# Kernel tuning notes

Hardware: AMD Instinct MI355X
Metric: run time of the kernel (lower is better)

## Reference

```python
import jax, jax.numpy as jnp
import numpy as np

NEG_SLOPE = 0.01  # torch nn.LeakyReLU default
N_NODES, N_EDGES, N_BATCH, L_PATH = 100000, 300000, 50000, 4
D_EMB, D_HID, N_HEADS = 128, 64, 8


def setup_inputs() -> dict:
    key = jax.random.key(0)
    ks = jax.random.split(key, 10)
    return {
        "batch_nodes": jax.random.randint(ks[0], (N_BATCH,), 0, N_NODES),
        "metapath_indices": jax.random.randint(ks[1], (N_EDGES, L_PATH), 0, N_NODES),
        "edge_dst": jax.random.randint(ks[2], (N_EDGES,), 0, N_NODES),
        "transformed_feature": jax.random.normal(ks[3], (N_NODES, D_EMB), jnp.float32),
        "W_i": jax.random.normal(ks[4], (D_HID, D_EMB), jnp.float32) * 0.05,
        "W_p": jax.random.normal(ks[5], (D_HID, D_EMB), jnp.float32) * 0.05,
        "attn": jax.random.normal(ks[6], (1, N_HEADS, D_HID), jnp.float32) * 0.05,
        "W_th": jax.random.normal(ks[7], (N_HEADS, N_HEADS), jnp.float32) * 0.3,
        "W_gate": jax.random.normal(ks[8], (1, D_HID), jnp.float32) * 0.1,
        "b_gate": jnp.zeros((1,), jnp.float32),
    }


def reference(batch_nodes, metapath_indices, edge_dst, transformed_feature,
              W_i, W_p, attn, W_th, W_gate, b_gate):
    N = transformed_feature.shape[0]
    # node_type_specific_agg for mtype==1: h_src/h_dst through linear_i, h_p1/h_p2 through linear_p
    membd = transformed_feature[metapath_indices]                      # [E, 4, D_emb]
    edata = (membd[:, 0] + membd[:, 3]) @ W_i.T \
          + (membd[:, 1] + membd[:, 2]) @ W_p.T                        # [E, D]
    E, D = edata.shape
    H = attn.shape[1]
    # cat([edata]*H, dim=1).view(-1, H, D) duplicates edata per head
    efeat = jnp.broadcast_to(edata[:, None, :], (E, H, D))             # [E, H, D]
    # talking-heads attention logits, leaky-relu
    logits = (efeat * attn).sum(-1) @ W_th.T                           # [E, H]
    logits = jax.nn.leaky_relu(logits, NEG_SLOPE)
    # dgl edge_softmax: per-dst-node, per-head softmax over incoming edges (stable)
    m = jax.ops.segment_max(logits, edge_dst, num_segments=N)          # [N, H]
    ex = jnp.exp(logits - m[edge_dst])                                 # [E, H]
    den = jax.ops.segment_sum(ex, edge_dst, num_segments=N)            # [N, H]
    a = ex / den[edge_dst]                                             # [E, H]  (dropout rate 0)
    # message passing: ft = efeature * a, summed per dst node
    msgs = (efeat * a[:, :, None]).reshape(E, H * D)
    node_ft = jax.ops.segment_sum(msgs, edge_dst, num_segments=N)      # [N, H*D]
    result = node_ft[batch_nodes].reshape(-1, H, D)                    # [B, H, D]
    # gated multi-head attention: gate = mean over batch of fc_gate(result)
    gate = jnp.mean(result @ W_gate.T + b_gate, axis=0)                # [H, 1]
    result = result * gate[None]                                       # [B, H, D]
    return result.reshape(-1, H * D)
```

## Files before the change

### kernel.cpp

```cpp
#include <hip/hip_runtime.h>
#include <cstdint>
#include <cstddef>


typedef __attribute__((ext_vector_type(8))) short bf16x8;
typedef __attribute__((ext_vector_type(4))) float f32x4;
typedef __attribute__((ext_vector_type(8))) unsigned short u16x8;

__device__ __forceinline__ unsigned short f2bf(float f) {
    unsigned u = __float_as_uint(f);
    unsigned r = u + 0x7fffu + ((u >> 16) & 1u);
    return (unsigned short)(r >> 16);
}
__device__ __forceinline__ float bf2f(unsigned short h) {
    return __uint_as_float((unsigned)h << 16);
}
__device__ __forceinline__ unsigned fenc(float f) {
    unsigned u = __float_as_uint(f);
    return (u & 0x80000000u) ? ~u : (u | 0x80000000u);
}
__device__ __forceinline__ float fdec(unsigned k) {
    unsigned u = (k & 0x80000000u) ? (k & 0x7fffffffu) : ~k;
    return __uint_as_float(u);
}

__global__ __launch_bounds__(256) void k_prep(
    const float* __restrict__ Wi, const float* __restrict__ Wp,
    const float* __restrict__ attn,
    unsigned short* __restrict__ Whi, unsigned short* __restrict__ Wlo,
    unsigned short* __restrict__ Phi, unsigned short* __restrict__ Plo,
    const int* __restrict__ batch_nodes, int* __restrict__ mult, int B) {
    int t = blockIdx.x * 256 + threadIdx.x;
    if (t < B) atomicAdd(&mult[batch_nodes[t]], 1);
    if (t < 16384) {
        int j = t & 7, L = (t >> 3) & 63, c = (t >> 9) & 7, s = t >> 12;
        int k = s * 32 + (L >> 4) * 8 + j;
        int n = c * 16 + (L & 15);
        float v = (n < 64) ? Wi[n * 128 + k] : Wp[(n - 64) * 128 + k];
        unsigned short h = f2bf(v);
        Whi[t] = h;
        Wlo[t] = f2bf(v - bf2f(h));
    } else if (t < 16384 + 2048) {
        int t2 = t - 16384;
        int j = t2 & 7, L = (t2 >> 3) & 63, s = t2 >> 9;
        int k = s * 32 + (L >> 4) * 8 + j;
        int i = L & 15;
        const float* Wsrc = (i < 8) ? Wi : Wp;
        const float* av = attn + (size_t)(i & 7) * 64;
        float v = 0.f;
#pragma unroll 8
        for (int d = 0; d < 64; ++d) v += av[d] * Wsrc[d * 128 + k];
        unsigned short h = f2bf(v);
        Phi[t2] = h;
        Plo[t2] = f2bf(v - bf2f(h));
    }
}

__global__ __launch_bounds__(256, 4) void k_dense(
    const float* __restrict__ feat, const unsigned short* __restrict__ Whi,
    const unsigned short* __restrict__ Wlo, const unsigned short* __restrict__ Phi,
    const unsigned short* __restrict__ Plo,
    const int* __restrict__ edge_dst, const int* __restrict__ mult,
    int* __restrict__ count, unsigned short* __restrict__ Ybf,
    float* __restrict__ P, int M, int E) {
    int t = threadIdx.x;

    {
        int e = blockIdx.x * 256 + t;
        if (e < E) {
            int d = edge_dst[e];
            if (mult[d] > 0) atomicAdd(&count[d], 1);
        }
    }

    int L = t & 63;
    int wave = t >> 6;
    int m = L & 15, q = L >> 4;
    int R0 = blockIdx.x * 64 + wave * 16;

    int rowc = R0 + m; if (rowc > M - 1) rowc = M - 1;
    const float* arow = feat + (size_t)rowc * 128;

    float4 av0[4], av1[4];
#pragma unroll
    for (int s = 0; s < 4; ++s) {
        const float4* ap = (const float4*)(arow + s * 32 + q * 8);
        av0[s] = ap[0];
        av1[s] = ap[1];
    }
    bf16x8 ahi[4], alo[4];
#pragma unroll
    for (int s = 0; s < 4; ++s) {
        float av[8] = {av0[s].x, av0[s].y, av0[s].z, av0[s].w,
                       av1[s].x, av1[s].y, av1[s].z, av1[s].w};
#pragma unroll
        for (int j = 0; j < 8; ++j) {
            unsigned short h = f2bf(av[j]);
            ahi[s][j] = (short)h;
            alo[s][j] = (short)f2bf(av[j] - bf2f(h));
        }
    }

    f32x4 acc[8];
#pragma unroll
    for (int c = 0; c < 8; ++c) acc[c] = (f32x4){0.f, 0.f, 0.f, 0.f};
    f32x4 accP = (f32x4){0.f, 0.f, 0.f, 0.f};

    const bf16x8* gh = (const bf16x8*)Whi;
    const bf16x8* gl = (const bf16x8*)Wlo;
    const bf16x8* ph = (const bf16x8*)Phi;
    const bf16x8* pl = (const bf16x8*)Plo;
#pragma unroll
    for (int s = 0; s < 4; ++s) {
#pragma unroll
        for (int c = 0; c < 8; ++c) {
            bf16x8 bh = gh[(s * 8 + c) * 64 + L];
            bf16x8 bl = gl[(s * 8 + c) * 64 + L];
            acc[c] = __builtin_amdgcn_mfma_f32_16x16x32_bf16(ahi[s], bh, acc[c], 0, 0, 0);
            acc[c] = __builtin_amdgcn_mfma_f32_16x16x32_bf16(ahi[s], bl, acc[c], 0, 0, 0);
            acc[c] = __builtin_amdgcn_mfma_f32_16x16x32_bf16(alo[s], bh, acc[c], 0, 0, 0);
        }
        {
            bf16x8 bh = ph[s * 64 + L];
            bf16x8 bl = pl[s * 64 + L];
            accP = __builtin_amdgcn_mfma_f32_16x16x32_bf16(ahi[s], bh, accP, 0, 0, 0);
            accP = __builtin_amdgcn_mfma_f32_16x16x32_bf16(ahi[s], bl, accP, 0, 0, 0);
            accP = __builtin_amdgcn_mfma_f32_16x16x32_bf16(alo[s], bh, accP, 0, 0, 0);
        }
    }

#pragma unroll
    for (int c = 0; c < 8; ++c) {
#pragma unroll
        for (int r = 0; r < 4; ++r) {
            int row = R0 + q * 4 + r;
            if (row < M) Ybf[(size_t)row * 128 + c * 16 + m] = f2bf(acc[c][r]);
        }
    }
#pragma unroll
    for (int r = 0; r < 4; ++r) {
        int row = R0 + q * 4 + r;
        if (row < M) P[(size_t)row * 16 + m] = accP[r];
    }
}

__global__ __launch_bounds__(256) void k_scan1(
    const int* __restrict__ count, int* __restrict__ excl, int* __restrict__ partials, int N) {
    __shared__ int lds[256];
    int t = threadIdx.x, i = blockIdx.x * 256 + t;
    int c = (i < N) ? count[i] : 0;
    lds[t] = c; __syncthreads();
    for (int o = 1; o < 256; o <<= 1) {
        int v = (t >= o) ? lds[t - o] : 0;
        __syncthreads(); lds[t] += v; __syncthreads();
    }
    if (i < N) excl[i] = lds[t] - c;
    if (t == 255) partials[blockIdx.x] = lds[255];
}

__global__ __launch_bounds__(256) void k_scan23(
    const int* __restrict__ excl, const int* __restrict__ partials,
    int* __restrict__ offsets, int* __restrict__ cursor, int N) {
    __shared__ int sacc[256];
    int bid = blockIdx.x, t = threadIdx.x;
    int s = 0;
    for (int j = t; j < bid; j += 256) s += partials[j];
    sacc[t] = s; __syncthreads();
#pragma unroll
    for (int o = 128; o > 0; o >>= 1) {
        if (t < o) sacc[t] += sacc[t + o];
        __syncthreads();
    }
    int boff = sacc[0];
    int i = bid * 256 + t;
    if (i < N) {
        int o = excl[i] + boff;
        offsets[i] = o; cursor[i] = o;
    }
    if (t == 0 && bid == gridDim.x - 1) offsets[N] = boff + partials[bid];
}

__global__ __launch_bounds__(256) void k_scatter_logits(
    const int* __restrict__ edge_dst, const int* __restrict__ mult,
    int* __restrict__ cursor, const int* __restrict__ mp,
    const float* __restrict__ P, const float* __restrict__ Wth,
    float* __restrict__ logits, int4* __restrict__ mpc,
    unsigned* __restrict__ mxkey, int E) {
    int e = blockIdx.x * 32 + (threadIdx.x >> 3);
    if (e >= E) return;
    int h = threadIdx.x & 7;
    int d = edge_dst[e];
    if (mult[d] == 0) return;
    int pos = 0;
    if (h == 0) pos = atomicAdd(&cursor[d], 1);
    int gbase = threadIdx.x & ~7;
    pos = __shfl(pos, gbase);
    int4 rows = *(const int4*)(mp + (size_t)e * 4);
    float s = P[(size_t)rows.x * 16 + h] + P[(size_t)rows.w * 16 + h]
            + P[(size_t)rows.y * 16 + 8 + h] + P[(size_t)rows.z * 16 + 8 + h];
    float l = 0.f;
#pragma unroll
    for (int j = 0; j < 8; ++j) {
        float sj = __shfl(s, gbase + j);
        l += Wth[h * 8 + j] * sj;
    }
    l = l > 0.f ? l : 0.01f * l;
    logits[(size_t)pos * 8 + h] = l;
    atomicMax(&mxkey[(size_t)d * 8 + h], fenc(l));
    if (h == 0) mpc[pos] = rows;
}

__global__ __launch_bounds__(256) void k_node_agg(
    const unsigned short* __restrict__ Ybf, const float* __restrict__ logits,
    const int4* __restrict__ mpc, const int* __restrict__ offsets,
    const int* __restrict__ mult, const unsigned* __restrict__ mxkey,
    const float* __restrict__ Wg,
    unsigned short* __restrict__ nftb, float* __restrict__ gate_part, int N) {
    int n = blockIdx.x * 4 + (threadIdx.x >> 6);
    int lane = threadIdx.x & 63;
    if (n >= N) return;
    int m = mult[n];
    if (m == 0) return;
    int beg = offsets[n], end = offsets[n + 1];

    float mx[8], den[8], acc[8];
#pragma unroll
    for (int h = 0; h < 8; ++h) {
        mx[h] = fdec(mxkey[(size_t)n * 8 + h]);
        den[h] = 0.f; acc[h] = 0.f;
    }

    for (int j = beg; j < end; ++j) {
        const float4* lp = (const float4*)(logits + (size_t)j * 8);
        float4 l0 = lp[0], l1 = lp[1];
        int4 rows = mpc[j];
        float ed = bf2f(Ybf[(size_t)rows.x * 128 + lane])
                 + bf2f(Ybf[(size_t)rows.w * 128 + lane])
                 + bf2f(Ybf[(size_t)rows.y * 128 + 64 + lane])
                 + bf2f(Ybf[(size_t)rows.z * 128 + 64 + lane]);
        float w0 = __expf(l0.x - mx[0]), w1 = __expf(l0.y - mx[1]);
        float w2 = __expf(l0.z - mx[2]), w3 = __expf(l0.w - mx[3]);
        float w4 = __expf(l1.x - mx[4]), w5 = __expf(l1.y - mx[5]);
        float w6 = __expf(l1.z - mx[6]), w7 = __expf(l1.w - mx[7]);
        den[0] += w0; den[1] += w1; den[2] += w2; den[3] += w3;
        den[4] += w4; den[5] += w5; den[6] += w6; den[7] += w7;
        acc[0] += w0 * ed; acc[1] += w1 * ed; acc[2] += w2 * ed; acc[3] += w3 * ed;
        acc[4] += w4 * ed; acc[5] += w5 * ed; acc[6] += w6 * ed; acc[7] += w7 * ed;
    }

#pragma unroll
    for (int h = 0; h < 8; ++h) {
        float r = (end > beg) ? 1.f / den[h] : 0.f;
        acc[h] *= r;
    }

    unsigned short* base = nftb + (size_t)n * 512;
#pragma unroll
    for (int h = 0; h < 8; ++h) base[h * 64 + lane] = f2bf(acc[h]);

    float wg = Wg[lane];
    float myg = 0.f;
#pragma unroll
    for (int h = 0; h < 8; ++h) {
        float p = acc[h] * wg;
#pragma unroll
        for (int o = 32; o > 0; o >>= 1) p += __shfl_xor(p, o);
        if (lane == h) myg = p;
    }
    if (lane < 8)
        atomicAdd(&gate_part[(blockIdx.x & 1023) * 8 + lane], (float)m * myg);
}

__global__ __launch_bounds__(256) void k_gatefinal(
    const float* __restrict__ gate_part, const float* __restrict__ b_gate,
    float* __restrict__ gate, int B) {
    __shared__ float lds[256];
    int t = threadIdx.x;
    int h = t & 7, g = t >> 3;
    float s = 0.f;
    for (int b = g; b < 1024; b += 32) s += gate_part[b * 8 + h];
    lds[t] = s; __syncthreads();
    if (t < 8) {
        float tot = 0.f;
        for (int gg = 0; gg < 32; ++gg) tot += lds[gg * 8 + t];
        gate[t] = tot / (float)B + b_gate[0];
    }
}

__global__ __launch_bounds__(256) void k_output(
    const unsigned short* __restrict__ nftb, const int* __restrict__ batch_nodes,
    const float* __restrict__ gate, float* __restrict__ out, int B) {
    int idx = blockIdx.x * 256 + threadIdx.x;
    int total = B * 64;
    if (idx >= total) return;
    int b = idx >> 6;
    int r = idx & 63;
    int h = r >> 3;
    int n = batch_nodes[b];
    u16x8 v = *(const u16x8*)(nftb + (size_t)n * 512 + r * 8);
    float g = gate[h];
    f32x4 o0, o1;
    o0[0] = bf2f(v[0]) * g; o0[1] = bf2f(v[1]) * g;
    o0[2] = bf2f(v[2]) * g; o0[3] = bf2f(v[3]) * g;
    o1[0] = bf2f(v[4]) * g; o1[1] = bf2f(v[5]) * g;
    o1[2] = bf2f(v[6]) * g; o1[3] = bf2f(v[7]) * g;
    f32x4* op = (f32x4*)(out + (size_t)idx * 8);
    __builtin_nontemporal_store(o0, op);
    __builtin_nontemporal_store(o1, op + 1);
}

extern "C" void kernel_launch(void* const* d_in, const int* in_sizes, int n_in,
                              void* d_out, int out_size, void* d_ws, size_t ws_size,
                              hipStream_t stream) {
    const int*   batch_nodes = (const int*)d_in[0];
    const int*   mp          = (const int*)d_in[1];
    const int*   edge_dst    = (const int*)d_in[2];
    const float* feat        = (const float*)d_in[3];
    const float* W_i         = (const float*)d_in[4];
    const float* W_p         = (const float*)d_in[5];
    const float* attn        = (const float*)d_in[6];
    const float* W_th        = (const float*)d_in[7];
    const float* W_gate      = (const float*)d_in[8];
    const float* b_gate      = (const float*)d_in[9];
    float* out = (float*)d_out;

    const int B = in_sizes[0];
    const int E = in_sizes[2];
    const int N = in_sizes[3] / 128;
    const int nb_scan = (N + 255) / 256;

    char* w = (char*)d_ws;
    auto alloc = [&](size_t bytes) -> void* {
        void* p = (void*)w;
        w += (bytes + 255) & ~(size_t)255;
        return p;
    };
    unsigned short* Whi = (unsigned short*)alloc(16384 * 2);
    unsigned short* Wlo = (unsigned short*)alloc(16384 * 2);
    unsigned short* Phi = (unsigned short*)alloc(2048 * 2);
    unsigned short* Plo = (unsigned short*)alloc(2048 * 2);
    unsigned short* Ybf = (unsigned short*)alloc((size_t)N * 128 * 2);
    float* P            = (float*)alloc((size_t)N * 16 * 4);
    float* logits       = (float*)alloc((size_t)E * 8 * 4);
    int4*  mpc          = (int4*)alloc((size_t)E * 16);
    size_t zero_bytes   = (size_t)N * 4 + (size_t)N * 4 + 1024 * 8 * 4
                        + (size_t)N * 8 * 4;
    int*   mult         = (int*)alloc(zero_bytes);
    int*   count        = mult + N;
    float* gate_part    = (float*)(count + N);
    unsigned* mxkey     = (unsigned*)(gate_part + 8192);
    int*   excl         = (int*)alloc((size_t)N * 4);
    int*   offsets      = (int*)alloc((size_t)(N + 1) * 4);
    int*   cursor       = (int*)alloc((size_t)N * 4);
    int*   partials     = (int*)alloc(512 * 4);
    unsigned short* nftb = (unsigned short*)alloc((size_t)N * 512 * 2);
    float* gate         = (float*)alloc(256);

    hipMemsetAsync(mult, 0, zero_bytes, stream);

    int prep_work = (B > 16384 + 2048) ? B : 16384 + 2048;
    k_prep<<<(prep_work + 255) / 256, 256, 0, stream>>>(W_i, W_p, attn,
                                                        Whi, Wlo, Phi, Plo,
                                                        batch_nodes, mult, B);
    k_dense<<<(N + 63) / 64, 256, 0, stream>>>(feat, Whi, Wlo, Phi, Plo,
                                               edge_dst, mult, count, Ybf, P, N, E);
    k_scan1<<<nb_scan, 256, 0, stream>>>(count, excl, partials, N);
    k_scan23<<<nb_scan, 256, 0, stream>>>(excl, partials, offsets, cursor, N);
    k_scatter_logits<<<(E + 31) / 32, 256, 0, stream>>>(edge_dst, mult, cursor,
                                                        mp, P, W_th, logits, mpc,
                                                        mxkey, E);
    k_node_agg<<<(N + 3) / 4, 256, 0, stream>>>(Ybf, logits, mpc, offsets, mult,
                                                mxkey, W_gate, nftb, gate_part, N);
    k_gatefinal<<<1, 256, 0, stream>>>(gate_part, b_gate, gate, B);
    k_output<<<(B * 64 + 255) / 256, 256, 0, stream>>>(nftb, batch_nodes, gate, out, B);
}
```

Baseline: 307.8 us.

## Split node aggregation across two wavefronts and fold gate finalize into output

Each destination node in the aggregation kernel is now handled by two wavefronts that stride over its incoming edges and combine partial sums through shared memory, doubling parallelism per node. The separate single-block gate reduction kernel is removed: every output block re-reduces a smaller 256-entry gate partial array itself, saving a launch. This adds a block-wide barrier and LDS traffic in aggregation, and redundant partial reduction work in every output block.

```diff
diff --git a/kernel.cpp b/kernel.cpp
--- a/kernel.cpp
+++ b/kernel.cpp
@@ -216,21 +216,28 @@
     const int* __restrict__ mult, const unsigned* __restrict__ mxkey,
     const float* __restrict__ Wg,
     unsigned short* __restrict__ nftb, float* __restrict__ gate_part, int N) {
-    int n = blockIdx.x * 4 + (threadIdx.x >> 6);
-    int lane = threadIdx.x & 63;
-    if (n >= N) return;
-    int m = mult[n];
-    if (m == 0) return;
-    int beg = offsets[n], end = offsets[n + 1];
+    __shared__ float sacc[2][8][64];
+    __shared__ float sden[2][8];
+    int t = threadIdx.x;
+    int pair = t >> 7;
+    int wp   = (t >> 6) & 1;
+    int lane = t & 63;
+    int n = blockIdx.x * 2 + pair;
+
+    int m = 0, beg = 0, end = 0;
+    bool active = false;
+    if (n < N) { m = mult[n]; active = (m > 0); }
 
     float mx[8], den[8], acc[8];
 #pragma unroll
-    for (int h = 0; h < 8; ++h) {
-        mx[h] = fdec(mxkey[(size_t)n * 8 + h]);
-        den[h] = 0.f; acc[h] = 0.f;
-    }
-
-    for (int j = beg; j < end; ++j) {
+    for (int h = 0; h < 8; ++h) { mx[h] = 0.f; den[h] = 0.f; acc[h] = 0.f; }
+    if (active) {
+        beg = offsets[n]; end = offsets[n + 1];
+#pragma unroll
+        for (int h = 0; h < 8; ++h) mx[h] = fdec(mxkey[(size_t)n * 8 + h]);
+    }
+
+    for (int j = beg + wp; j < end; j += 2) {
         const float4* lp = (const float4*)(logits + (size_t)j * 8);
         float4 l0 = lp[0], l1 = lp[1];
         int4 rows = mpc[j];
@@ -248,49 +255,63 @@
         acc[4] += w4 * ed; acc[5] += w5 * ed; acc[6] += w6 * ed; acc[7] += w7 * ed;
     }
 
-#pragma unroll
-    for (int h = 0; h < 8; ++h) {
-        float r = (end > beg) ? 1.f / den[h] : 0.f;
-        acc[h] *= r;
-    }
-
-    unsigned short* base = nftb + (size_t)n * 512;
-#pragma unroll
-    for (int h = 0; h < 8; ++h) base[h * 64 + lane] = f2bf(acc[h]);
-
-    float wg = Wg[lane];
-    float myg = 0.f;
-#pragma unroll
-    for (int h = 0; h < 8; ++h) {
-        float p = acc[h] * wg;
-#pragma unroll
-        for (int o = 32; o > 0; o >>= 1) p += __shfl_xor(p, o);
-        if (lane == h) myg = p;
-    }
-    if (lane < 8)
-        atomicAdd(&gate_part[(blockIdx.x & 1023) * 8 + lane], (float)m * myg);
-}
-
-__global__ __launch_bounds__(256) void k_gatefinal(
-    const float* __restrict__ gate_part, const float* __restrict__ b_gate,
-    float* __restrict__ gate, int B) {
-    __shared__ float lds[256];
-    int t = threadIdx.x;
-    int h = t & 7, g = t >> 3;
-    float s = 0.f;
-    for (int b = g; b < 1024; b += 32) s += gate_part[b * 8 + h];
-    lds[t] = s; __syncthreads();
-    if (t < 8) {
-        float tot = 0.f;
-        for (int gg = 0; gg < 32; ++gg) tot += lds[gg * 8 + t];
-        gate[t] = tot / (float)B + b_gate[0];
+    if (wp == 1) {
+#pragma unroll
+        for (int h = 0; h < 8; ++h) sacc[pair][h][lane] = acc[h];
+        float dv = 0.f;
+#pragma unroll
+        for (int h = 0; h < 8; ++h) dv = (lane == h) ? den[h] : dv;
+        if (lane < 8) sden[pair][lane] = dv;
+    }
+    __syncthreads();
+
+    if (wp == 0 && active) {
+#pragma unroll
+        for (int h = 0; h < 8; ++h) {
+            acc[h] += sacc[pair][h][lane];
+            den[h] += sden[pair][h];
+            float r = (end > beg) ? 1.f / den[h] : 0.f;
+            acc[h] *= r;
+        }
+
+        unsigned short* base = nftb + (size_t)n * 512;
+#pragma unroll
+        for (int h = 0; h < 8; ++h) base[h * 64 + lane] = f2bf(acc[h]);
+
+        float wg = Wg[lane];
+        float myg = 0.f;
+#pragma unroll
+        for (int h = 0; h < 8; ++h) {
+            float p = acc[h] * wg;
+#pragma unroll
+            for (int o = 32; o > 0; o >>= 1) p += __shfl_xor(p, o);
+            if (lane == h) myg = p;
+        }
+        if (lane < 8)
+            atomicAdd(&gate_part[(blockIdx.x & 255) * 8 + lane], (float)m * myg);
     }
 }
 
 __global__ __launch_bounds__(256) void k_output(
     const unsigned short* __restrict__ nftb, const int* __restrict__ batch_nodes,
-    const float* __restrict__ gate, float* __restrict__ out, int B) {
-    int idx = blockIdx.x * 256 + threadIdx.x;
+    const float* __restrict__ gate_part, const float* __restrict__ b_gate,
+    float* __restrict__ out, int B) {
+    __shared__ float lds[256];
+    __shared__ float sg[8];
+    int t = threadIdx.x;
+    {
+        int h = t & 7, g = t >> 3;
+        float s = 0.f;
+        for (int b = g; b < 256; b += 32) s += gate_part[b * 8 + h];
+        lds[t] = s; __syncthreads();
+        if (t < 8) {
+            float tot = 0.f;
+            for (int gg = 0; gg < 32; ++gg) tot += lds[gg * 8 + t];
+            sg[t] = tot / (float)B + b_gate[0];
+        }
+        __syncthreads();
+    }
+    int idx = blockIdx.x * 256 + t;
     int total = B * 64;
     if (idx >= total) return;
     int b = idx >> 6;
@@ -298,7 +319,7 @@
     int h = r >> 3;
     int n = batch_nodes[b];
     u16x8 v = *(const u16x8*)(nftb + (size_t)n * 512 + r * 8);
-    float g = gate[h];
+    float g = sg[h];
     f32x4 o0, o1;
     o0[0] = bf2f(v[0]) * g; o0[1] = bf2f(v[1]) * g;
     o0[2] = bf2f(v[2]) * g; o0[3] = bf2f(v[3]) * g;
@@ -343,18 +364,17 @@
     float* P            = (float*)alloc((size_t)N * 16 * 4);
     float* logits       = (float*)alloc((size_t)E * 8 * 4);
     int4*  mpc          = (int4*)alloc((size_t)E * 16);
-    size_t zero_bytes   = (size_t)N * 4 + (size_t)N * 4 + 1024 * 8 * 4
+    size_t zero_bytes   = (size_t)N * 4 + (size_t)N * 4 + 256 * 8 * 4
                         + (size_t)N * 8 * 4;
     int*   mult         = (int*)alloc(zero_bytes);
     int*   count        = mult + N;
     float* gate_part    = (float*)(count + N);
-    unsigned* mxkey     = (unsigned*)(gate_part + 8192);
+    unsigned* mxkey     = (unsigned*)(gate_part + 256 * 8);
     int*   excl         = (int*)alloc((size_t)N * 4);
     int*   offsets      = (int*)alloc((size_t)(N + 1) * 4);
     int*   cursor       = (int*)alloc((size_t)N * 4);
     int*   partials     = (int*)alloc(512 * 4);
     unsigned short* nftb = (unsigned short*)alloc((size_t)N * 512 * 2);
-    float* gate         = (float*)alloc(256);
 
     hipMemsetAsync(mult, 0, zero_bytes, stream);
 
@@ -369,8 +389,8 @@
     k_scatter_logits<<<(E + 31) / 32, 256, 0, stream>>>(edge_dst, mult, cursor,
                                                         mp, P, W_th, logits, mpc,
                                                         mxkey, E);
-    k_node_agg<<<(N + 3) / 4, 256, 0, stream>>>(Ybf, logits, mpc, offsets, mult,
+    k_node_agg<<<(N + 1) / 2, 256, 0, stream>>>(Ybf, logits, mpc, offsets, mult,
                                                 mxkey, W_gate, nftb, gate_part, N);
-    k_gatefinal<<<1, 256, 0, stream>>>(gate_part, b_gate, gate, B);
-    k_output<<<(B * 64 + 255) / 256, 256, 0, stream>>>(nftb, batch_nodes, gate, out, B);
-}
+    k_output<<<(B * 64 + 255) / 256, 256, 0, stream>>>(nftb, batch_nodes,
+                                                       gate_part, b_gate, out, B);
+}
```

After: 313.5 us. About the same (+1.9%).

## Persistent node-aggregation waves and fold gate finalisation into output kernel

Applied to the files above, without the earlier changes.

The node aggregation kernel becomes grid-stride over nodes with a fixed 2048-block grid. Each wave accumulates its gate partials in registers and issues a single reduction and atomic at the end, instead of one shuffle reduction and atomic per node. The separate single-block gate-final kernel is removed, and every output block now recomputes the gate from 256 partial slots in shared memory. This saves a launch and many atomics, at the cost of redundant per-block gate reduction and possible load imbalance from the fixed grid.

```diff
diff --git a/kernel.cpp b/kernel.cpp
--- a/kernel.cpp
+++ b/kernel.cpp
@@ -216,81 +216,91 @@
     const int* __restrict__ mult, const unsigned* __restrict__ mxkey,
     const float* __restrict__ Wg,
     unsigned short* __restrict__ nftb, float* __restrict__ gate_part, int N) {
-    int n = blockIdx.x * 4 + (threadIdx.x >> 6);
     int lane = threadIdx.x & 63;
-    if (n >= N) return;
-    int m = mult[n];
-    if (m == 0) return;
-    int beg = offsets[n], end = offsets[n + 1];
-
-    float mx[8], den[8], acc[8];
+    int gwave = blockIdx.x * 4 + (threadIdx.x >> 6);
+    int nwaves = gridDim.x * 4;
+    float wg = Wg[lane];
+
+    float gp[8];
+#pragma unroll
+    for (int h = 0; h < 8; ++h) gp[h] = 0.f;
+
+    for (int n = gwave; n < N; n += nwaves) {
+        int m = mult[n];
+        if (m == 0) continue;
+        int beg = offsets[n], end = offsets[n + 1];
+
+        float mx[8], den[8], acc[8];
+#pragma unroll
+        for (int h = 0; h < 8; ++h) {
+            mx[h] = fdec(mxkey[(size_t)n * 8 + h]);
+            den[h] = 0.f; acc[h] = 0.f;
+        }
+
+        for (int j = beg; j < end; ++j) {
+            const float4* lp = (const float4*)(logits + (size_t)j * 8);
+            float4 l0 = lp[0], l1 = lp[1];
+            int4 rows = mpc[j];
+            float ed = bf2f(Ybf[(size_t)rows.x * 128 + lane])
+                     + bf2f(Ybf[(size_t)rows.w * 128 + lane])
+                     + bf2f(Ybf[(size_t)rows.y * 128 + 64 + lane])
+                     + bf2f(Ybf[(size_t)rows.z * 128 + 64 + lane]);
+            float w0 = __expf(l0.x - mx[0]), w1 = __expf(l0.y - mx[1]);
+            float w2 = __expf(l0.z - mx[2]), w3 = __expf(l0.w - mx[3]);
+            float w4 = __expf(l1.x - mx[4]), w5 = __expf(l1.y - mx[5]);
+            float w6 = __expf(l1.z - mx[6]), w7 = __expf(l1.w - mx[7]);
+            den[0] += w0; den[1] += w1; den[2] += w2; den[3] += w3;
+            den[4] += w4; den[5] += w5; den[6] += w6; den[7] += w7;
+            acc[0] += w0 * ed; acc[1] += w1 * ed; acc[2] += w2 * ed; acc[3] += w3 * ed;
+            acc[4] += w4 * ed; acc[5] += w5 * ed; acc[6] += w6 * ed; acc[7] += w7 * ed;
+        }
+
+#pragma unroll
+        for (int h = 0; h < 8; ++h) {
+            float r = (end > beg) ? 1.f / den[h] : 0.f;
+            acc[h] *= r;
+        }
+
+        unsigned short* base = nftb + (size_t)n * 512;
+#pragma unroll
+        for (int h = 0; h < 8; ++h) base[h * 64 + lane] = f2bf(acc[h]);
+
+#pragma unroll
+        for (int h = 0; h < 8; ++h) gp[h] += (float)m * acc[h];
+    }
+
+    float myg = 0.f;
 #pragma unroll
     for (int h = 0; h < 8; ++h) {
-        mx[h] = fdec(mxkey[(size_t)n * 8 + h]);
-        den[h] = 0.f; acc[h] = 0.f;
-    }
-
-    for (int j = beg; j < end; ++j) {
-        const float4* lp = (const float4*)(logits + (size_t)j * 8);
-        float4 l0 = lp[0], l1 = lp[1];
-        int4 rows = mpc[j];
-        float ed = bf2f(Ybf[(size_t)rows.x * 128 + lane])
-                 + bf2f(Ybf[(size_t)rows.w * 128 + lane])
-                 + bf2f(Ybf[(size_t)rows.y * 128 + 64 + lane])
-                 + bf2f(Ybf[(size_t)rows.z * 128 + 64 + lane]);
-        float w0 = __expf(l0.x - mx[0]), w1 = __expf(l0.y - mx[1]);
-        float w2 = __expf(l0.z - mx[2]), w3 = __expf(l0.w - mx[3]);
-        float w4 = __expf(l1.x - mx[4]), w5 = __expf(l1.y - mx[5]);
-        float w6 = __expf(l1.z - mx[6]), w7 = __expf(l1.w - mx[7]);
-        den[0] += w0; den[1] += w1; den[2] += w2; den[3] += w3;
-        den[4] += w4; den[5] += w5; den[6] += w6; den[7] += w7;
-        acc[0] += w0 * ed; acc[1] += w1 * ed; acc[2] += w2 * ed; acc[3] += w3 * ed;
-        acc[4] += w4 * ed; acc[5] += w5 * ed; acc[6] += w6 * ed; acc[7] += w7 * ed;
-    }
-
-#pragma unroll
-    for (int h = 0; h < 8; ++h) {
-        float r = (end > beg) ? 1.f / den[h] : 0.f;
-        acc[h] *= r;
-    }
-
-    unsigned short* base = nftb + (size_t)n * 512;
-#pragma unroll
-    for (int h = 0; h < 8; ++h) base[h * 64 + lane] = f2bf(acc[h]);
-
-    float wg = Wg[lane];
-    float myg = 0.f;
-#pragma unroll
-    for (int h = 0; h < 8; ++h) {
-        float p = acc[h] * wg;
+        float p = gp[h] * wg;
 #pragma unroll
         for (int o = 32; o > 0; o >>= 1) p += __shfl_xor(p, o);
         if (lane == h) myg = p;
     }
     if (lane < 8)
-        atomicAdd(&gate_part[(blockIdx.x & 1023) * 8 + lane], (float)m * myg);
-}
-
-__global__ __launch_bounds__(256) void k_gatefinal(
-    const float* __restrict__ gate_part, const float* __restrict__ b_gate,
-    float* __restrict__ gate, int B) {
-    __shared__ float lds[256];
-    int t = threadIdx.x;
-    int h = t & 7, g = t >> 3;
-    float s = 0.f;
-    for (int b = g; b < 1024; b += 32) s += gate_part[b * 8 + h];
-    lds[t] = s; __syncthreads();
-    if (t < 8) {
-        float tot = 0.f;
-        for (int gg = 0; gg < 32; ++gg) tot += lds[gg * 8 + t];
-        gate[t] = tot / (float)B + b_gate[0];
-    }
+        atomicAdd(&gate_part[(blockIdx.x & 255) * 8 + lane], myg);
 }
 
 __global__ __launch_bounds__(256) void k_output(
     const unsigned short* __restrict__ nftb, const int* __restrict__ batch_nodes,
-    const float* __restrict__ gate, float* __restrict__ out, int B) {
-    int idx = blockIdx.x * 256 + threadIdx.x;
+    const float* __restrict__ gate_part, const float* __restrict__ b_gate,
+    float* __restrict__ out, int B) {
+    __shared__ float lds[256];
+    __shared__ float sg[8];
+    int t = threadIdx.x;
+    {
+        int h = t & 7, g = t >> 3;
+        float s = 0.f;
+        for (int b = g; b < 256; b += 32) s += gate_part[b * 8 + h];
+        lds[t] = s; __syncthreads();
+        if (t < 8) {
+            float tot = 0.f;
+            for (int gg = 0; gg < 32; ++gg) tot += lds[gg * 8 + t];
+            sg[t] = tot / (float)B + b_gate[0];
+        }
+        __syncthreads();
+    }
+    int idx = blockIdx.x * 256 + t;
     int total = B * 64;
     if (idx >= total) return;
     int b = idx >> 6;
@@ -298,7 +308,7 @@
     int h = r >> 3;
     int n = batch_nodes[b];
     u16x8 v = *(const u16x8*)(nftb + (size_t)n * 512 + r * 8);
-    float g = gate[h];
+    float g = sg[h];
     f32x4 o0, o1;
     o0[0] = bf2f(v[0]) * g; o0[1] = bf2f(v[1]) * g;
     o0[2] = bf2f(v[2]) * g; o0[3] = bf2f(v[3]) * g;
@@ -343,18 +353,17 @@
     float* P            = (float*)alloc((size_t)N * 16 * 4);
     float* logits       = (float*)alloc((size_t)E * 8 * 4);
     int4*  mpc          = (int4*)alloc((size_t)E * 16);
-    size_t zero_bytes   = (size_t)N * 4 + (size_t)N * 4 + 1024 * 8 * 4
+    size_t zero_bytes   = (size_t)N * 4 + (size_t)N * 4 + 256 * 8 * 4
                         + (size_t)N * 8 * 4;
     int*   mult         = (int*)alloc(zero_bytes);
     int*   count        = mult + N;
     float* gate_part    = (float*)(count + N);
-    unsigned* mxkey     = (unsigned*)(gate_part + 8192);
+    unsigned* mxkey     = (unsigned*)(gate_part + 256 * 8);
     int*   excl         = (int*)alloc((size_t)N * 4);
     int*   offsets      = (int*)alloc((size_t)(N + 1) * 4);
     int*   cursor       = (int*)alloc((size_t)N * 4);
     int*   partials     = (int*)alloc(512 * 4);
     unsigned short* nftb = (unsigned short*)alloc((size_t)N * 512 * 2);
-    float* gate         = (float*)alloc(256);
 
     hipMemsetAsync(mult, 0, zero_bytes, stream);
 
@@ -369,8 +378,8 @@
     k_scatter_logits<<<(E + 31) / 32, 256, 0, stream>>>(edge_dst, mult, cursor,
                                                         mp, P, W_th, logits, mpc,
                                                         mxkey, E);
-    k_node_agg<<<(N + 3) / 4, 256, 0, stream>>>(Ybf, logits, mpc, offsets, mult,
-                                                mxkey, W_gate, nftb, gate_part, N);
-    k_gatefinal<<<1, 256, 0, stream>>>(gate_part, b_gate, gate, B);
-    k_output<<<(B * 64 + 255) / 256, 256, 0, stream>>>(nftb, batch_nodes, gate, out, B);
-}
+    k_node_agg<<<2048, 256, 0, stream>>>(Ybf, logits, mpc, offsets, mult,
+                                         mxkey, W_gate, nftb, gate_part, N);
+    k_output<<<(B * 64 + 255) / 256, 256, 0, stream>>>(nftb, batch_nodes,
+                                                       gate_part, b_gate, out, B);
+}
```

Measured after the change: 303.4 us. No clear change (-1.4%).
